# Kernel tuning notes

Measured on AMD Instinct MI355X. Metric: run time of the kernel, lower is better.

Reference implementation:

```python
import jax, jax.numpy as jnp
import numpy as np

N_POINTS = 131072
N_ANCHORS = 2048


def setup_inputs() -> dict:
    key = jax.random.key(0)
    k1, k2, k3, k4 = jax.random.split(key, 4)
    locations3d = jax.random.normal(k1, (N_POINTS, 3), dtype=jnp.float32)
    anchor_locations3d = jax.random.normal(k2, (N_ANCHORS, 3), dtype=jnp.float32)
    anchor_coeffs = jax.random.normal(k3, (N_ANCHORS,), dtype=jnp.float32)
    # per-anchor widths, kept strictly positive in [0.1, 1.0)
    anchor_parameters = jax.random.uniform(k4, (N_ANCHORS,), dtype=jnp.float32) * 0.9 + 0.1
    return {
        "locations3d": locations3d,
        "anchor_locations3d": anchor_locations3d,
        "anchor_coeffs": anchor_coeffs,
        "anchor_parameters": anchor_parameters,
    }


def potential_operator(locations3d, anchor_locations3d, anchor_parameters):
    # Pairwise squared distances via the expanded form (avoids [N,M,3] intermediate):
    x_sq = jnp.sum(locations3d * locations3d, axis=-1, keepdims=True)          # [N,1]
    a_sq = jnp.sum(anchor_locations3d * anchor_locations3d, axis=-1)            # [M]
    cross = locations3d @ anchor_locations3d.T                                  # [N,M]
    sqdist = x_sq + a_sq[None, :] - 2.0 * cross
    sqdist = jnp.maximum(sqdist, 0.0)
    inv_two_w2 = 0.5 / (anchor_parameters * anchor_parameters)                  # [M]
    return jnp.exp(-sqdist * inv_two_w2[None, :])                               # [N,M]


def reference(locations3d, anchor_locations3d, anchor_coeffs, anchor_parameters):
    K = potential_operator(locations3d, anchor_locations3d, anchor_parameters)  # [N,M]
    return K @ anchor_coeffs                                                    # [N]
```

## Files before the change

kernel.cpp:

```cpp
#include <hip/hip_runtime.h>

#define N_POINTS  131072
#define N_ANCHORS 2048
#define CHUNKS    16
#define M_PER     (N_ANCHORS / CHUNKS)
#define THREADS   256
#define PTS       4
#define PT_STRIDE (N_POINTS / PTS)
#define LOG2E     1.4426950408889634f

typedef float v2f __attribute__((ext_vector_type(2)));

struct __align__(64) Anchor {
    v2f r0, r1, r2, q, sp, cf;
    v2f pad0, pad1;
};

__global__ void precompute_anchors(const float* __restrict__ aloc,
                                   const float* __restrict__ coeffs,
                                   const float* __restrict__ params,
                                   Anchor* __restrict__ A) {
    int m = blockIdx.x * blockDim.x + threadIdx.x;
    if (m >= N_ANCHORS) return;
    const float a0 = aloc[3 * m + 0];
    const float a1 = aloc[3 * m + 1];
    const float a2 = aloc[3 * m + 2];
    const float w  = params[m];
    const float sp = -(0.5f * LOG2E) / (w * w);
    const float r0 = -2.0f * sp * a0;
    const float r1 = -2.0f * sp * a1;
    const float r2 = -2.0f * sp * a2;
    const float q  = sp * (a0 * a0 + a1 * a1 + a2 * a2);
    const float cf = coeffs[m];
    Anchor out;
    out.r0 = (v2f){r0, r0};  out.r1 = (v2f){r1, r1};
    out.r2 = (v2f){r2, r2};  out.q  = (v2f){q, q};
    out.sp = (v2f){sp, sp};  out.cf = (v2f){cf, cf};
    out.pad0 = (v2f){0.f, 0.f}; out.pad1 = (v2f){0.f, 0.f};
    A[m] = out;
}

__global__ __launch_bounds__(256, 8) void linear_potential_main(
    const float* __restrict__ xloc,
    const Anchor* __restrict__ anchors,
    float* __restrict__ out)
{
    const int t   = threadIdx.x;
    const int tid = blockIdx.x * THREADS + t;
    const int n0 = tid;
    const int n1 = tid + PT_STRIDE;
    const int n2 = tid + 2 * PT_STRIDE;
    const int n3 = tid + 3 * PT_STRIDE;

    const v2f xa = { xloc[3 * n0 + 0], xloc[3 * n1 + 0] };
    const v2f ya = { xloc[3 * n0 + 1], xloc[3 * n1 + 1] };
    const v2f za = { xloc[3 * n0 + 2], xloc[3 * n1 + 2] };
    const v2f xb = { xloc[3 * n2 + 0], xloc[3 * n3 + 0] };
    const v2f yb = { xloc[3 * n2 + 1], xloc[3 * n3 + 1] };
    const v2f zb = { xloc[3 * n2 + 2], xloc[3 * n3 + 2] };

    const v2f ssa = __builtin_elementwise_fma(xa, xa,
                    __builtin_elementwise_fma(ya, ya, za * za));
    const v2f ssb = __builtin_elementwise_fma(xb, xb,
                    __builtin_elementwise_fma(yb, yb, zb * zb));

    v2f acca = { 0.0f, 0.0f };
    v2f accb = { 0.0f, 0.0f };

    const Anchor* __restrict__ ach = anchors + blockIdx.y * M_PER;

    #pragma unroll 4
    for (int mm = 0; mm < M_PER; ++mm) {
        const v2f r0 = ach[mm].r0;
        const v2f r1 = ach[mm].r1;
        const v2f r2 = ach[mm].r2;
        const v2f q  = ach[mm].q;
        const v2f sp = ach[mm].sp;
        const v2f cf = ach[mm].cf;

        v2f arga = __builtin_elementwise_fma(sp, ssa, q);
        arga     = __builtin_elementwise_fma(r0, xa, arga);
        arga     = __builtin_elementwise_fma(r1, ya, arga);
        arga     = __builtin_elementwise_fma(r2, za, arga);

        v2f argb = __builtin_elementwise_fma(sp, ssb, q);
        argb     = __builtin_elementwise_fma(r0, xb, argb);
        argb     = __builtin_elementwise_fma(r1, yb, argb);
        argb     = __builtin_elementwise_fma(r2, zb, argb);

        v2f ea = { __builtin_amdgcn_exp2f(arga.x), __builtin_amdgcn_exp2f(arga.y) };
        v2f eb = { __builtin_amdgcn_exp2f(argb.x), __builtin_amdgcn_exp2f(argb.y) };

        acca = __builtin_elementwise_fma(cf, ea, acca);
        accb = __builtin_elementwise_fma(cf, eb, accb);
    }

    atomicAdd(&out[n0], acca.x);
    atomicAdd(&out[n1], acca.y);
    atomicAdd(&out[n2], accb.x);
    atomicAdd(&out[n3], accb.y);
}

extern "C" void kernel_launch(void* const* d_in, const int* in_sizes, int n_in,
                              void* d_out, int out_size, void* d_ws, size_t ws_size,
                              hipStream_t stream) {
    const float* xloc   = (const float*)d_in[0];
    const float* aloc   = (const float*)d_in[1];
    const float* coeffs = (const float*)d_in[2];
    const float* params = (const float*)d_in[3];
    float* out = (float*)d_out;

    Anchor* A = (Anchor*)d_ws;

    hipMemsetAsync(d_out, 0, N_POINTS * sizeof(float), stream);

    precompute_anchors<<<dim3(N_ANCHORS / 256), dim3(256), 0, stream>>>(
        aloc, coeffs, params, A);

    linear_potential_main<<<dim3(N_POINTS / (THREADS * PTS), CHUNKS),
                            dim3(THREADS), 0, stream>>>(
        xloc, A, out);
}
```

Before: 102.9 us.

## Fuse anchor precompute into main kernel via LDS and double anchor chunks

Removes the separate anchor-precompute kernel: each block now computes its own slice of anchor constants into shared memory, then runs the inner loop from LDS instead of global/scalar loads. The anchor split doubles from 16 to 32 chunks, giving more blocks with shorter loops, and the unroll factor rises to 8. This saves a kernel launch and global traffic, at the cost of redundant per-block precompute, a barrier, and twice as many atomic adds to the output.

Measured after the change: 98.70 us. -4.1%, faster.

```diff
diff --git a/kernel.cpp b/kernel.cpp
--- a/kernel.cpp
+++ b/kernel.cpp
@@ -2,7 +2,7 @@
 
 #define N_POINTS  131072
 #define N_ANCHORS 2048
-#define CHUNKS    16
+#define CHUNKS    32
 #define M_PER     (N_ANCHORS / CHUNKS)
 #define THREADS   256
 #define PTS       4
@@ -11,41 +11,43 @@
 
 typedef float v2f __attribute__((ext_vector_type(2)));
 
-struct __align__(64) Anchor {
+struct __align__(16) AnchorLds {
     v2f r0, r1, r2, q, sp, cf;
     v2f pad0, pad1;
 };
 
-__global__ void precompute_anchors(const float* __restrict__ aloc,
-                                   const float* __restrict__ coeffs,
-                                   const float* __restrict__ params,
-                                   Anchor* __restrict__ A) {
-    int m = blockIdx.x * blockDim.x + threadIdx.x;
-    if (m >= N_ANCHORS) return;
-    const float a0 = aloc[3 * m + 0];
-    const float a1 = aloc[3 * m + 1];
-    const float a2 = aloc[3 * m + 2];
-    const float w  = params[m];
-    const float sp = -(0.5f * LOG2E) / (w * w);
-    const float r0 = -2.0f * sp * a0;
-    const float r1 = -2.0f * sp * a1;
-    const float r2 = -2.0f * sp * a2;
-    const float q  = sp * (a0 * a0 + a1 * a1 + a2 * a2);
-    const float cf = coeffs[m];
-    Anchor out;
-    out.r0 = (v2f){r0, r0};  out.r1 = (v2f){r1, r1};
-    out.r2 = (v2f){r2, r2};  out.q  = (v2f){q, q};
-    out.sp = (v2f){sp, sp};  out.cf = (v2f){cf, cf};
-    out.pad0 = (v2f){0.f, 0.f}; out.pad1 = (v2f){0.f, 0.f};
-    A[m] = out;
-}
-
 __global__ __launch_bounds__(256, 8) void linear_potential_main(
     const float* __restrict__ xloc,
-    const Anchor* __restrict__ anchors,
+    const float* __restrict__ aloc,
+    const float* __restrict__ coeffs,
+    const float* __restrict__ params,
     float* __restrict__ out)
 {
-    const int t   = threadIdx.x;
+    __shared__ AnchorLds sA[M_PER];
+
+    const int t = threadIdx.x;
+
+    if (t < M_PER) {
+        const int m  = blockIdx.y * M_PER + t;
+        const float a0 = aloc[3 * m + 0];
+        const float a1 = aloc[3 * m + 1];
+        const float a2 = aloc[3 * m + 2];
+        const float w  = params[m];
+        const float sp = -(0.5f * LOG2E) / (w * w);
+        const float r0 = -2.0f * sp * a0;
+        const float r1 = -2.0f * sp * a1;
+        const float r2 = -2.0f * sp * a2;
+        const float q  = sp * (a0 * a0 + a1 * a1 + a2 * a2);
+        const float cf = coeffs[m];
+        sA[t].r0 = (v2f){r0, r0};
+        sA[t].r1 = (v2f){r1, r1};
+        sA[t].r2 = (v2f){r2, r2};
+        sA[t].q  = (v2f){q,  q};
+        sA[t].sp = (v2f){sp, sp};
+        sA[t].cf = (v2f){cf, cf};
+    }
+    __syncthreads();
+
     const int tid = blockIdx.x * THREADS + t;
     const int n0 = tid;
     const int n1 = tid + PT_STRIDE;
@@ -67,16 +69,14 @@
     v2f acca = { 0.0f, 0.0f };
     v2f accb = { 0.0f, 0.0f };
 
-    const Anchor* __restrict__ ach = anchors + blockIdx.y * M_PER;
-
-    #pragma unroll 4
+    #pragma unroll 8
     for (int mm = 0; mm < M_PER; ++mm) {
-        const v2f r0 = ach[mm].r0;
-        const v2f r1 = ach[mm].r1;
-        const v2f r2 = ach[mm].r2;
-        const v2f q  = ach[mm].q;
-        const v2f sp = ach[mm].sp;
-        const v2f cf = ach[mm].cf;
+        const v2f r0 = sA[mm].r0;
+        const v2f r1 = sA[mm].r1;
+        const v2f r2 = sA[mm].r2;
+        const v2f q  = sA[mm].q;
+        const v2f sp = sA[mm].sp;
+        const v2f cf = sA[mm].cf;
 
         v2f arga = __builtin_elementwise_fma(sp, ssa, q);
         arga     = __builtin_elementwise_fma(r0, xa, arga);
@@ -110,14 +110,9 @@
     const float* params = (const float*)d_in[3];
     float* out = (float*)d_out;
 
-    Anchor* A = (Anchor*)d_ws;
-
     hipMemsetAsync(d_out, 0, N_POINTS * sizeof(float), stream);
-
-    precompute_anchors<<<dim3(N_ANCHORS / 256), dim3(256), 0, stream>>>(
-        aloc, coeffs, params, A);
 
     linear_potential_main<<<dim3(N_POINTS / (THREADS * PTS), CHUNKS),
                             dim3(THREADS), 0, stream>>>(
-        xloc, A, out);
+        xloc, aloc, coeffs, params, out);
 }
```
